# Optimization experiments

Hardware: AMD Instinct MI355X
Metric: run time of the kernel (lower is better)

Reference implementation:

```python
import jax, jax.numpy as jnp
import numpy as np

HEADS = 2
HID = 128
IN_DIM = 128
OUT_DIM = 1
N_NODES = 50000
NEG_SLOPE = 0.2  # PyG GATConv default
EPS = 1e-16


def setup_inputs() -> dict:
    key = jax.random.key(0)
    ks = jax.random.split(key, 16)
    N, E = N_NODES, 800000
    x = jax.random.normal(ks[0], (N, IN_DIM), dtype=jnp.float32)
    edge_index = jax.random.randint(ks[1], (2, E), 0, N, dtype=jnp.int32)
    s = 0.1
    # GATConv 1: in=128 -> heads=2, out=128 per head
    W1 = jax.random.normal(ks[2], (IN_DIM, HEADS * HID), dtype=jnp.float32) * s
    a_src1 = jax.random.normal(ks[3], (HEADS, HID), dtype=jnp.float32) * s
    a_dst1 = jax.random.normal(ks[4], (HEADS, HID), dtype=jnp.float32) * s
    b1 = jnp.zeros((HEADS * HID,), dtype=jnp.float32)
    # GATConv 2: in=256 -> heads=2, out=128 per head
    W2 = jax.random.normal(ks[5], (HEADS * HID, HEADS * HID), dtype=jnp.float32) * s
    a_src2 = jax.random.normal(ks[6], (HEADS, HID), dtype=jnp.float32) * s
    a_dst2 = jax.random.normal(ks[7], (HEADS, HID), dtype=jnp.float32) * s
    b2 = jnp.zeros((HEADS * HID,), dtype=jnp.float32)
    # post_mp: Linear(256,128) -> Dropout -> Linear(128,1)
    Wp1 = jax.random.normal(ks[8], (HEADS * HID, HID), dtype=jnp.float32) * s
    bp1 = jnp.zeros((HID,), dtype=jnp.float32)
    Wp2 = jax.random.normal(ks[9], (HID, OUT_DIM), dtype=jnp.float32) * s
    bp2 = jnp.zeros((OUT_DIM,), dtype=jnp.float32)
    return {"x": x, "edge_index": edge_index,
            "W1": W1, "a_src1": a_src1, "a_dst1": a_dst1, "b1": b1,
            "W2": W2, "a_src2": a_src2, "a_dst2": a_dst2, "b2": b2,
            "Wp1": Wp1, "bp1": bp1, "Wp2": Wp2, "bp2": bp2}


def gat_conv(x, src, dst, W, a_src, a_dst, b, num_nodes):
    """PyG-style GATConv (concat=True). src/dst already include self-loops."""
    N = num_nodes
    h = (x @ W).reshape(N, HEADS, HID)                        # [N,H,C]
    alpha_s = jnp.einsum('nhc,hc->nh', h, a_src)              # [N,H]
    alpha_d = jnp.einsum('nhc,hc->nh', h, a_dst)              # [N,H]
    e = jax.nn.leaky_relu(alpha_s[src] + alpha_d[dst], NEG_SLOPE)  # [E,H]
    # segment softmax over destination node
    emax = jax.ops.segment_max(e, dst, num_segments=N)        # [N,H]
    emax = jnp.where(jnp.isfinite(emax), emax, 0.0)
    w = jnp.exp(e - emax[dst])                                # [E,H]
    denom = jax.ops.segment_sum(w, dst, num_segments=N)       # [N,H]
    alpha = w / (denom[dst] + EPS)                            # [E,H]
    out = jax.ops.segment_sum(h[src] * alpha[:, :, None], dst, num_segments=N)
    return out.reshape(N, HEADS * HID) + b


def reference(x, edge_index, W1, a_src1, a_dst1, b1, W2, a_src2, a_dst2, b2,
              Wp1, bp1, Wp2, bp2):
    N = x.shape[0]
    loops = jnp.arange(N, dtype=edge_index.dtype)
    src = jnp.concatenate([edge_index[0], loops])
    dst = jnp.concatenate([edge_index[1], loops])
    h = gat_conv(x, src, dst, W1, a_src1, a_dst1, b1, N)
    h = jax.nn.relu(h)  # dropout is identity in eval mode
    h = gat_conv(h, src, dst, W2, a_src2, a_dst2, b2, N)
    h = jax.nn.relu(h)
    h = h @ Wp1 + bp1
    h = h @ Wp2 + bp2
    return jax.nn.sigmoid(h)
```

## Files before the change

kernel.cpp:

```cpp
#include <hip/hip_runtime.h>

#define HID 128
#define C2 256
#define NEG 0.2f
#define L2E 1.44269504088896340736f

typedef __bf16 v8bf __attribute__((ext_vector_type(8)));
typedef float  v4f  __attribute__((ext_vector_type(4)));
typedef float  v2f  __attribute__((ext_vector_type(2)));
typedef unsigned short us8 __attribute__((ext_vector_type(8)));

__device__ __forceinline__ float bf2f(unsigned short u) {
    union { float f; unsigned int i; } v; v.i = ((unsigned int)u) << 16; return v.f;
}
__device__ __forceinline__ unsigned short f2bf(float f) {
    union { float f; unsigned int i; } v; v.f = f;
    unsigned int r = v.i + 0x7FFFu + ((v.i >> 16) & 1u);
    return (unsigned short)(r >> 16);
}
__device__ __forceinline__ float lrelu(float x) { return x > 0.f ? x : NEG * x; }

__device__ __forceinline__ void packB_body(const float* __restrict__ W,
                                           unsigned short* __restrict__ out,
                                           int K, int N, int idx) {
    int ksteps = K >> 5;
    int total = (N >> 4) * ksteps * 64;
    if (idx >= total) return;
    int lane = idx & 63;
    int rest = idx >> 6;
    int tt = rest / ksteps, k0 = rest - tt * ksteps;
    int n = (tt >> 3) * 128 + (lane & 15) * 8 + (tt & 7);
    int kb = k0 * 32 + (lane >> 4) * 8;
    us8 v;
#pragma unroll
    for (int j = 0; j < 8; ++j) v[j] = f2bf(W[(size_t)(kb + j) * N + n]);
    *(us8*)(out + (size_t)idx * 8) = v;
}

__global__ __launch_bounds__(256) void prep_kernel(const float* __restrict__ W1, unsigned short* W1p,
                                                   const float* __restrict__ W2, unsigned short* W2p,
                                                   const float* __restrict__ Wp1, unsigned short* Wp1p,
                                                   const int* __restrict__ ei, int* __restrict__ cnt,
                                                   int* __restrict__ rank, int E,
                                                   int b1, int b2, int b3) {
    int b = blockIdx.x;
    if (b < b1) { packB_body(W1, W1p, HID, C2, b * 256 + threadIdx.x); return; }
    b -= b1;
    if (b < b2) { packB_body(W2, W2p, C2, C2, b * 256 + threadIdx.x); return; }
    b -= b2;
    if (b < b3) { packB_body(Wp1, Wp1p, C2, HID, b * 256 + threadIdx.x); return; }
    b -= b3;
    int i = b * 256 + threadIdx.x;
    if (i >= E) return;
    int d = ei[E + i];
    rank[i] = atomicAdd(&cnt[d], 1);
}

__global__ __launch_bounds__(256) void scanA(const int* __restrict__ cnt, int* __restrict__ rs,
                                             int* __restrict__ part, int N) {
    __shared__ int s[256];
    int t = threadIdx.x, i = blockIdx.x * 256 + t;
    int v = (i < N) ? cnt[i] : 0;
    s[t] = v; __syncthreads();
    for (int off = 1; off < 256; off <<= 1) {
        int x = (t >= off) ? s[t - off] : 0;
        __syncthreads();
        s[t] += x;
        __syncthreads();
    }
    if (i < N) rs[i] = s[t] - v;
    if (t == 255) part[blockIdx.x] = s[255];
}

__global__ __launch_bounds__(256) void scanB(int* __restrict__ part, int n) {
    __shared__ int s[256];
    int t = threadIdx.x;
    int v = (t < n) ? part[t] : 0;
    s[t] = v; __syncthreads();
    for (int off = 1; off < 256; off <<= 1) {
        int x = (t >= off) ? s[t - off] : 0;
        __syncthreads();
        s[t] += x;
        __syncthreads();
    }
    if (t < n) part[t] = s[t] - v;
}

__global__ void scanC(int* __restrict__ rs, const int* __restrict__ part, int N, int E) {
    int i = blockIdx.x * 256 + threadIdx.x;
    if (i < N) rs[i] += part[blockIdx.x];
    if (i == 0) rs[N] = E;
}

template<bool AFP32, int G, int KSTEPS>
__global__ __launch_bounds__(256) void gemm_alpha(const void* __restrict__ Av,
                                                  const unsigned short* __restrict__ Bp,
                                                  const float* __restrict__ asrc,
                                                  const float* __restrict__ adst,
                                                  float* __restrict__ asd,
                                                  unsigned char* __restrict__ C,
                                                  int M, int N, int gemmBlocks,
                                                  const int* __restrict__ ei,
                                                  const int* __restrict__ rs,
                                                  const int* __restrict__ rank,
                                                  int* __restrict__ csr, int E) {
    if (blockIdx.x >= gemmBlocks) {
        int i = (blockIdx.x - gemmBlocks) * 256 + threadIdx.x;
        if (i < E) {
            int s = ei[i], d = ei[E + i];
            csr[rs[d] + rank[i]] = s;
        }
        return;
    }
    constexpr int K = KSTEPS * 32;
    int ngrp = N >> 7;
    int mtiles = M >> 4;
    int w = (blockIdx.x << 2) + (threadIdx.x >> 6);
    int groups = (mtiles + G - 1) / G;
    int mp = w / ngrp, g = w - mp * ngrp;
    if (mp >= groups) return;
    int lane = threadIdx.x & 63;
    int l16 = lane & 15, quad = lane >> 4;
    int mt0 = mp * G;

    int mrow[G];
#pragma unroll
    for (int gi = 0; gi < G; ++gi) {
        int mt = mt0 + gi;
        mrow[gi] = (mt < mtiles ? mt : mtiles - 1) * 16 + l16;
    }

    const unsigned short* Bf = Bp + ((size_t)(g * 8) * KSTEPS << 9) + lane * 8;
    v4f acc[G][8];
#pragma unroll
    for (int gi = 0; gi < G; ++gi)
#pragma unroll
        for (int t = 0; t < 8; ++t) acc[gi][t] = (v4f){0, 0, 0, 0};

#pragma unroll
    for (int k0 = 0; k0 < KSTEPS; ++k0) {
        v8bf bfr[8];
#pragma unroll
        for (int t = 0; t < 8; ++t)
            bfr[t] = *(const v8bf*)(Bf + ((size_t)(t * KSTEPS + k0) << 9));
        v8bf a[G];
        if (AFP32) {
            const float* A = (const float*)Av;
#pragma unroll
            for (int gi = 0; gi < G; ++gi) {
                const float* p = A + (size_t)mrow[gi] * K + k0 * 32 + quad * 8;
                float4 u0 = *(const float4*)p, u1 = *(const float4*)(p + 4);
                a[gi][0]=(__bf16)u0.x; a[gi][1]=(__bf16)u0.y; a[gi][2]=(__bf16)u0.z; a[gi][3]=(__bf16)u0.w;
                a[gi][4]=(__bf16)u1.x; a[gi][5]=(__bf16)u1.y; a[gi][6]=(__bf16)u1.z; a[gi][7]=(__bf16)u1.w;
            }
        } else {
            const unsigned short* A = (const unsigned short*)Av;
#pragma unroll
            for (int gi = 0; gi < G; ++gi)
                a[gi] = *(const v8bf*)(A + (size_t)mrow[gi] * K + k0 * 32 + quad * 8);
        }
#pragma unroll
        for (int t = 0; t < 8; ++t)
#pragma unroll
            for (int gi = 0; gi < G; ++gi)
                acc[gi][t] = __builtin_amdgcn_mfma_f32_16x16x32_bf16(a[gi], bfr[t], acc[gi][t], 0, 0, 0);
    }

    int n0 = g << 7;
    int cb = n0 + l16 * 8;
    float sv[8], dv[8];
#pragma unroll
    for (int t = 0; t < 8; ++t) {
        sv[t] = asrc[cb + t];
        dv[t] = adst[cb + t];
    }
#pragma unroll
    for (int gi = 0; gi < G; ++gi) {
        int mt = mt0 + gi;
        if (mt >= mtiles) break;
        int row0 = mt * 16 + quad * 4;
#pragma unroll
        for (int r = 0; r < 4; ++r) {
            float sa = 0.f, sd = 0.f;
#pragma unroll
            for (int t = 0; t < 8; ++t) {
                sa += acc[gi][t][r] * sv[t];
                sd += acc[gi][t][r] * dv[t];
            }
            unsigned int w0 = __builtin_amdgcn_cvt_pk_fp8_f32(acc[gi][0][r], acc[gi][1][r], 0, false);
            w0 = __builtin_amdgcn_cvt_pk_fp8_f32(acc[gi][2][r], acc[gi][3][r], w0, true);
            unsigned int w1 = __builtin_amdgcn_cvt_pk_fp8_f32(acc[gi][4][r], acc[gi][5][r], 0, false);
            w1 = __builtin_amdgcn_cvt_pk_fp8_f32(acc[gi][6][r], acc[gi][7][r], w1, true);
            *(uint2*)(C + (size_t)(row0 + r) * N + cb) = (uint2){w0, w1};
#pragma unroll
            for (int off = 8; off; off >>= 1) {
                sa += __shfl_xor(sa, off);
                sd += __shfl_xor(sd, off);
            }
            if (l16 == 0) {
                int row = row0 + r;
                asd[(size_t)row * 4 + g]     = sa * L2E;
                asd[(size_t)row * 4 + 2 + g] = sd * L2E;
            }
        }
    }
}

__global__ __launch_bounds__(256) void agg_kernel(const int* __restrict__ rs,
                                                  const int* __restrict__ csr,
                                                  const unsigned char* __restrict__ h,
                                                  const float* __restrict__ asd,
                                                  const float* __restrict__ bias,
                                                  unsigned short* __restrict__ out, int N) {
    int d = blockIdx.x * 4 + (threadIdx.x >> 6);
    if (d >= N) return;
    int lane = threadIdx.x & 63;
    int beg = rs[d], end = rs[d + 1];
    int e4 = lane >> 4;
    int sub = lane & 15;
    int head = sub >> 3;
    int l32 = lane & 31;
    int whead = lane >> 5;
    float adh0 = asd[(size_t)d * 4 + 2];
    float adh1 = asd[(size_t)d * 4 + 3];
    float adh  = head  ? adh1 : adh0;
    float wadh = whead ? adh1 : adh0;
    int cbase = sub * 16;
    const unsigned char* hc = h + cbase;
    v2f acc[8];
#pragma unroll
    for (int j = 0; j < 8; ++j) acc[j] = (v2f){0, 0};
    float den = 0.f;
    for (int c0 = beg; c0 < end; c0 += 32) {
        int ce = c0 + l32;
        bool av = ce < end;
        int s_w = csr[av ? ce : end - 1];
        float e_w = lrelu(asd[(size_t)s_w * 4 + whead] + wadh);
        float w_w = av ? __builtin_amdgcn_exp2f(e_w) : 0.f;
        int rem = end - c0; if (rem > 32) rem = 32;
        int iters = (rem + 3) >> 2;
#pragma unroll 2
        for (int it = 0; it < iters; ++it) {
            int j = (it << 2) + e4;
            int   s   = __shfl(s_w, j);
            float wgt = __shfl(w_w, j + (head << 5));
            den += wgt;
            uint4 u = *(const uint4*)(hc + ((size_t)s << 8));
            v2f w2 = {wgt, wgt};
            acc[0] += w2 * __builtin_amdgcn_cvt_pk_f32_fp8(u.x, false);
            acc[1] += w2 * __builtin_amdgcn_cvt_pk_f32_fp8(u.x, true);
            acc[2] += w2 * __builtin_amdgcn_cvt_pk_f32_fp8(u.y, false);
            acc[3] += w2 * __builtin_amdgcn_cvt_pk_f32_fp8(u.y, true);
            acc[4] += w2 * __builtin_amdgcn_cvt_pk_f32_fp8(u.z, false);
            acc[5] += w2 * __builtin_amdgcn_cvt_pk_f32_fp8(u.z, true);
            acc[6] += w2 * __builtin_amdgcn_cvt_pk_f32_fp8(u.w, false);
            acc[7] += w2 * __builtin_amdgcn_cvt_pk_f32_fp8(u.w, true);
        }
    }
    float a[16];
#pragma unroll
    for (int j = 0; j < 8; ++j) { a[2 * j] = acc[j].x; a[2 * j + 1] = acc[j].y; }
#pragma unroll
    for (int j = 0; j < 16; ++j) a[j] += __shfl_xor(a[j], 16);
#pragma unroll
    for (int j = 0; j < 16; ++j) a[j] += __shfl_xor(a[j], 32);
    den += __shfl_xor(den, 16);
    den += __shfl_xor(den, 32);
    if (e4 == 0) {
        float wS = __builtin_amdgcn_exp2f(lrelu(asd[(size_t)d * 4 + head] + adh));
        uint4 u = *(const uint4*)(hc + (size_t)d * C2);
        v2f p;
        p = __builtin_amdgcn_cvt_pk_f32_fp8(u.x, false); a[0]  += wS * p.x; a[1]  += wS * p.y;
        p = __builtin_amdgcn_cvt_pk_f32_fp8(u.x, true);  a[2]  += wS * p.x; a[3]  += wS * p.y;
        p = __builtin_amdgcn_cvt_pk_f32_fp8(u.y, false); a[4]  += wS * p.x; a[5]  += wS * p.y;
        p = __builtin_amdgcn_cvt_pk_f32_fp8(u.y, true);  a[6]  += wS * p.x; a[7]  += wS * p.y;
        p = __builtin_amdgcn_cvt_pk_f32_fp8(u.z, false); a[8]  += wS * p.x; a[9]  += wS * p.y;
        p = __builtin_amdgcn_cvt_pk_f32_fp8(u.z, true);  a[10] += wS * p.x; a[11] += wS * p.y;
        p = __builtin_amdgcn_cvt_pk_f32_fp8(u.w, false); a[12] += wS * p.x; a[13] += wS * p.y;
        p = __builtin_amdgcn_cvt_pk_f32_fp8(u.w, true);  a[14] += wS * p.x; a[15] += wS * p.y;
        float rden = 1.f / (den + wS + 1e-16f);
        us8 o0, o1;
#pragma unroll
        for (int j = 0; j < 8; ++j) o0[j] = f2bf(fmaxf(a[j] * rden + bias[cbase + j], 0.f));
#pragma unroll
        for (int j = 0; j < 8; ++j) o1[j] = f2bf(fmaxf(a[8 + j] * rden + bias[cbase + 8 + j], 0.f));
        *(us8*)(out + (size_t)d * C2 + cbase) = o0;
        *(us8*)(out + (size_t)d * C2 + cbase + 8) = o1;
    }
}

template<int G, int KSTEPS>
__global__ __launch_bounds__(256) void gemm_final(const unsigned short* __restrict__ A,
                                                  const unsigned short* __restrict__ Bp,
                                                  const float* __restrict__ bp1,
                                                  const float* __restrict__ wp2,
                                                  const float* __restrict__ bp2,
                                                  float* __restrict__ out,
                                                  int M) {
    constexpr int K = KSTEPS * 32;
    int mtiles = M >> 4;
    int groups = (mtiles + G - 1) / G;
    int mp = (blockIdx.x << 2) + (threadIdx.x >> 6);
    if (mp >= groups) return;
    int lane = threadIdx.x & 63;
    int l16 = lane & 15, quad = lane >> 4;

    int mrow[G];
#pragma unroll
    for (int gi = 0; gi < G; ++gi) {
        int mt = mp * G + gi;
        mrow[gi] = (mt < mtiles ? mt : mtiles - 1) * 16 + l16;
    }

    const unsigned short* Bf = Bp + lane * 8;
    v4f acc[G][8];
#pragma unroll
    for (int gi = 0; gi < G; ++gi)
#pragma unroll
        for (int t = 0; t < 8; ++t) acc[gi][t] = (v4f){0, 0, 0, 0};
#pragma unroll
    for (int k0 = 0; k0 < KSTEPS; ++k0) {
        v8bf bfr[8];
#pragma unroll
        for (int t = 0; t < 8; ++t)
            bfr[t] = *(const v8bf*)(Bf + ((size_t)(t * KSTEPS + k0) << 9));
        v8bf a[G];
#pragma unroll
        for (int gi = 0; gi < G; ++gi)
            a[gi] = *(const v8bf*)(A + (size_t)mrow[gi] * K + k0 * 32 + quad * 8);
#pragma unroll
        for (int t = 0; t < 8; ++t)
#pragma unroll
            for (int gi = 0; gi < G; ++gi)
                acc[gi][t] = __builtin_amdgcn_mfma_f32_16x16x32_bf16(a[gi], bfr[t], acc[gi][t], 0, 0, 0);
    }
    int cb = l16 * 8;
    float wv8[8], bv[8];
#pragma unroll
    for (int t = 0; t < 8; ++t) {
        wv8[t] = wp2[cb + t];
        bv[t] = bp1[cb + t];
    }
    float bias2 = bp2[0];
#pragma unroll
    for (int gi = 0; gi < G; ++gi) {
        int mt = mp * G + gi;
        if (mt >= mtiles) break;
        int row0 = mt * 16 + quad * 4;
#pragma unroll
        for (int r = 0; r < 4; ++r) {
            float s = 0.f;
#pragma unroll
            for (int t = 0; t < 8; ++t) s += (acc[gi][t][r] + bv[t]) * wv8[t];
#pragma unroll
            for (int off = 8; off; off >>= 1) s += __shfl_xor(s, off);
            if (l16 == 0) {
                float xv = s + bias2;
                out[row0 + r] = 1.f / (1.f + __expf(-xv));
            }
        }
    }
}

extern "C" void kernel_launch(void* const* d_in, const int* in_sizes, int n_in,
                              void* d_out, int out_size, void* d_ws, size_t ws_size,
                              hipStream_t stream) {
    const float* x   = (const float*)d_in[0];
    const int*   ei  = (const int*)d_in[1];
    const float* W1  = (const float*)d_in[2];
    const float* as1 = (const float*)d_in[3];
    const float* ad1 = (const float*)d_in[4];
    const float* b1  = (const float*)d_in[5];
    const float* W2  = (const float*)d_in[6];
    const float* as2 = (const float*)d_in[7];
    const float* ad2 = (const float*)d_in[8];
    const float* b2  = (const float*)d_in[9];
    const float* Wp1 = (const float*)d_in[10];
    const float* bp1 = (const float*)d_in[11];
    const float* Wp2 = (const float*)d_in[12];
    const float* bp2 = (const float*)d_in[13];
    float* out = (float*)d_out;

    int NN = in_sizes[0] / HID;
    int E  = in_sizes[1] / 2;

    char* ws = (char*)d_ws;
    size_t off = 0;
    auto alloc = [&](size_t bytes) -> char* {
        char* p = ws + off;
        off += (bytes + 255) & ~(size_t)255;
        return p;
    };
    unsigned char*  bufH = (unsigned char*)alloc((size_t)NN * C2);
    unsigned short* bufO = (unsigned short*)alloc((size_t)NN * C2 * 2);
    float* asd = (float*)alloc((size_t)NN * 4 * sizeof(float));
    int* rs    = (int*)alloc((size_t)(NN + 1) * 4);
    int* cnt   = (int*)alloc((size_t)NN * 4);
    int* rank  = (int*)alloc((size_t)E * 4);
    int* csr   = (int*)alloc((size_t)E * 4);
    int* part  = (int*)alloc(1024);
    unsigned short* W1p  = (unsigned short*)alloc((size_t)HID * C2 * 2);
    unsigned short* W2p  = (unsigned short*)alloc((size_t)C2 * C2 * 2);
    unsigned short* Wp1p = (unsigned short*)alloc((size_t)C2 * HID * 2);

    int nchunk = (NN + 255) / 256;
    int eblk   = (E + 255) / 256;

    int pb1 = (HID * C2 / 8 + 255) / 256;
    int pb2 = (C2 * C2 / 8 + 255) / 256;
    int pb3 = (C2 * HID / 8 + 255) / 256;
    hipMemsetAsync(cnt, 0, (size_t)NN * 4, stream);
    prep_kernel<<<pb1 + pb2 + pb3 + eblk, 256, 0, stream>>>(W1, W1p, W2, W2p, Wp1, Wp1p,
                                                            ei, cnt, rank, E, pb1, pb2, pb3);
    scanA<<<nchunk, 256, 0, stream>>>(cnt, rs, part, NN);
    scanB<<<1, 256, 0, stream>>>(part, nchunk);
    scanC<<<nchunk, 256, 0, stream>>>(rs, part, NN, E);

    const int G = 2;
    int mtiles = NN / 16;
    int groups = (mtiles + G - 1) / G;
    int gemmBlocks = (groups * 2 + 3) / 4;
    int aggGrid = (NN + 3) / 4;

    gemm_alpha<true, G, 4><<<gemmBlocks + eblk, 256, 0, stream>>>(x, W1p, as1, ad1, asd, bufH,
                                                                  NN, C2, gemmBlocks,
                                                                  ei, rs, rank, csr, E);
    agg_kernel<<<aggGrid, 256, 0, stream>>>(rs, csr, bufH, asd, b1, bufO, NN);
    gemm_alpha<false, G, 8><<<gemmBlocks, 256, 0, stream>>>(bufO, W2p, as2, ad2, asd, bufH,
                                                            NN, C2, gemmBlocks,
                                                            nullptr, nullptr, nullptr, nullptr, 0);
    agg_kernel<<<aggGrid, 256, 0, stream>>>(rs, csr, bufH, asd, b2, bufO, NN);
    gemm_final<G, 8><<<(groups + 3) / 4, 256, 0, stream>>>(bufO, Wp1p, bp1, Wp2, bp2, out, NN);
}
```

Before: 305.9 us.

## Use 16 threads per destination node in GAT aggregation instead of a wavefront

The aggregation kernel now assigns 16 threads per destination node (16 nodes per block) instead of one 64-lane wavefront per node. Each thread walks the whole edge list serially, computing its head's edge weight directly, so the shuffle-based weight broadcast and cross-lane reduction are gone. This cuts redundant lanes and shuffle overhead for low-degree nodes (average degree about 17). In exchange there is less memory-level parallelism per node, per-edge index and score loads are repeated by all 16 threads, and divergence within a wavefront grows because four nodes of different degree share it.

```diff
diff --git a/kernel.cpp b/kernel.cpp
--- a/kernel.cpp
+++ b/kernel.cpp
@@ -212,81 +212,60 @@
                                                   const float* __restrict__ asd,
                                                   const float* __restrict__ bias,
                                                   unsigned short* __restrict__ out, int N) {
-    int d = blockIdx.x * 4 + (threadIdx.x >> 6);
+    int tid = threadIdx.x;
+    int grp = tid >> 4;
+    int sub = tid & 15;
+    int d = blockIdx.x * 16 + grp;
     if (d >= N) return;
-    int lane = threadIdx.x & 63;
+    int head = sub >> 3;
     int beg = rs[d], end = rs[d + 1];
-    int e4 = lane >> 4;
-    int sub = lane & 15;
-    int head = sub >> 3;
-    int l32 = lane & 31;
-    int whead = lane >> 5;
-    float adh0 = asd[(size_t)d * 4 + 2];
-    float adh1 = asd[(size_t)d * 4 + 3];
-    float adh  = head  ? adh1 : adh0;
-    float wadh = whead ? adh1 : adh0;
+    float adh = asd[(size_t)d * 4 + 2 + head];
     int cbase = sub * 16;
     const unsigned char* hc = h + cbase;
     v2f acc[8];
 #pragma unroll
     for (int j = 0; j < 8; ++j) acc[j] = (v2f){0, 0};
     float den = 0.f;
-    for (int c0 = beg; c0 < end; c0 += 32) {
-        int ce = c0 + l32;
-        bool av = ce < end;
-        int s_w = csr[av ? ce : end - 1];
-        float e_w = lrelu(asd[(size_t)s_w * 4 + whead] + wadh);
-        float w_w = av ? __builtin_amdgcn_exp2f(e_w) : 0.f;
-        int rem = end - c0; if (rem > 32) rem = 32;
-        int iters = (rem + 3) >> 2;
 #pragma unroll 2
-        for (int it = 0; it < iters; ++it) {
-            int j = (it << 2) + e4;
-            int   s   = __shfl(s_w, j);
-            float wgt = __shfl(w_w, j + (head << 5));
-            den += wgt;
-            uint4 u = *(const uint4*)(hc + ((size_t)s << 8));
-            v2f w2 = {wgt, wgt};
-            acc[0] += w2 * __builtin_amdgcn_cvt_pk_f32_fp8(u.x, false);
-            acc[1] += w2 * __builtin_amdgcn_cvt_pk_f32_fp8(u.x, true);
-            acc[2] += w2 * __builtin_amdgcn_cvt_pk_f32_fp8(u.y, false);
-            acc[3] += w2 * __builtin_amdgcn_cvt_pk_f32_fp8(u.y, true);
-            acc[4] += w2 * __builtin_amdgcn_cvt_pk_f32_fp8(u.z, false);
-            acc[5] += w2 * __builtin_amdgcn_cvt_pk_f32_fp8(u.z, true);
-            acc[6] += w2 * __builtin_amdgcn_cvt_pk_f32_fp8(u.w, false);
-            acc[7] += w2 * __builtin_amdgcn_cvt_pk_f32_fp8(u.w, true);
-        }
-    }
-    float a[16];
-#pragma unroll
-    for (int j = 0; j < 8; ++j) { a[2 * j] = acc[j].x; a[2 * j + 1] = acc[j].y; }
-#pragma unroll
-    for (int j = 0; j < 16; ++j) a[j] += __shfl_xor(a[j], 16);
-#pragma unroll
-    for (int j = 0; j < 16; ++j) a[j] += __shfl_xor(a[j], 32);
-    den += __shfl_xor(den, 16);
-    den += __shfl_xor(den, 32);
-    if (e4 == 0) {
-        float wS = __builtin_amdgcn_exp2f(lrelu(asd[(size_t)d * 4 + head] + adh));
-        uint4 u = *(const uint4*)(hc + (size_t)d * C2);
-        v2f p;
-        p = __builtin_amdgcn_cvt_pk_f32_fp8(u.x, false); a[0]  += wS * p.x; a[1]  += wS * p.y;
-        p = __builtin_amdgcn_cvt_pk_f32_fp8(u.x, true);  a[2]  += wS * p.x; a[3]  += wS * p.y;
-        p = __builtin_amdgcn_cvt_pk_f32_fp8(u.y, false); a[4]  += wS * p.x; a[5]  += wS * p.y;
-        p = __builtin_amdgcn_cvt_pk_f32_fp8(u.y, true);  a[6]  += wS * p.x; a[7]  += wS * p.y;
-        p = __builtin_amdgcn_cvt_pk_f32_fp8(u.z, false); a[8]  += wS * p.x; a[9]  += wS * p.y;
-        p = __builtin_amdgcn_cvt_pk_f32_fp8(u.z, true);  a[10] += wS * p.x; a[11] += wS * p.y;
-        p = __builtin_amdgcn_cvt_pk_f32_fp8(u.w, false); a[12] += wS * p.x; a[13] += wS * p.y;
-        p = __builtin_amdgcn_cvt_pk_f32_fp8(u.w, true);  a[14] += wS * p.x; a[15] += wS * p.y;
-        float rden = 1.f / (den + wS + 1e-16f);
-        us8 o0, o1;
-#pragma unroll
-        for (int j = 0; j < 8; ++j) o0[j] = f2bf(fmaxf(a[j] * rden + bias[cbase + j], 0.f));
-#pragma unroll
-        for (int j = 0; j < 8; ++j) o1[j] = f2bf(fmaxf(a[8 + j] * rden + bias[cbase + 8 + j], 0.f));
-        *(us8*)(out + (size_t)d * C2 + cbase) = o0;
-        *(us8*)(out + (size_t)d * C2 + cbase + 8) = o1;
-    }
+    for (int i = beg; i < end; ++i) {
+        int s = csr[i];
+        float wgt = __builtin_amdgcn_exp2f(lrelu(asd[(size_t)s * 4 + head] + adh));
+        den += wgt;
+        uint4 u = *(const uint4*)(hc + ((size_t)s << 8));
+        v2f w2 = {wgt, wgt};
+        acc[0] += w2 * __builtin_amdgcn_cvt_pk_f32_fp8(u.x, false);
+        acc[1] += w2 * __builtin_amdgcn_cvt_pk_f32_fp8(u.x, true);
+        acc[2] += w2 * __builtin_amdgcn_cvt_pk_f32_fp8(u.y, false);
+        acc[3] += w2 * __builtin_amdgcn_cvt_pk_f32_fp8(u.y, true);
+        acc[4] += w2 * __builtin_amdgcn_cvt_pk_f32_fp8(u.z, false);
+        acc[5] += w2 * __builtin_amdgcn_cvt_pk_f32_fp8(u.z, true);
+        acc[6] += w2 * __builtin_amdgcn_cvt_pk_f32_fp8(u.w, false);
+        acc[7] += w2 * __builtin_amdgcn_cvt_pk_f32_fp8(u.w, true);
+    }
+    float wS = __builtin_amdgcn_exp2f(lrelu(asd[(size_t)d * 4 + head] + adh));
+    {
+        uint4 u = *(const uint4*)(hc + ((size_t)d << 8));
+        v2f wsv = {wS, wS};
+        acc[0] += wsv * __builtin_amdgcn_cvt_pk_f32_fp8(u.x, false);
+        acc[1] += wsv * __builtin_amdgcn_cvt_pk_f32_fp8(u.x, true);
+        acc[2] += wsv * __builtin_amdgcn_cvt_pk_f32_fp8(u.y, false);
+        acc[3] += wsv * __builtin_amdgcn_cvt_pk_f32_fp8(u.y, true);
+        acc[4] += wsv * __builtin_amdgcn_cvt_pk_f32_fp8(u.z, false);
+        acc[5] += wsv * __builtin_amdgcn_cvt_pk_f32_fp8(u.z, true);
+        acc[6] += wsv * __builtin_amdgcn_cvt_pk_f32_fp8(u.w, false);
+        acc[7] += wsv * __builtin_amdgcn_cvt_pk_f32_fp8(u.w, true);
+    }
+    float rden = 1.f / (den + wS + 1e-16f);
+    us8 o0, o1;
+#pragma unroll
+    for (int j = 0; j < 4; ++j) {
+        o0[2 * j]     = f2bf(fmaxf(acc[j].x * rden + bias[cbase + 2 * j], 0.f));
+        o0[2 * j + 1] = f2bf(fmaxf(acc[j].y * rden + bias[cbase + 2 * j + 1], 0.f));
+        o1[2 * j]     = f2bf(fmaxf(acc[4 + j].x * rden + bias[cbase + 8 + 2 * j], 0.f));
+        o1[2 * j + 1] = f2bf(fmaxf(acc[4 + j].y * rden + bias[cbase + 8 + 2 * j + 1], 0.f));
+    }
+    *(us8*)(out + (size_t)d * C2 + cbase) = o0;
+    *(us8*)(out + (size_t)d * C2 + cbase + 8) = o1;
 }
 
 template<int G, int KSTEPS>
@@ -420,7 +399,7 @@
     int mtiles = NN / 16;
     int groups = (mtiles + G - 1) / G;
     int gemmBlocks = (groups * 2 + 3) / 4;
-    int aggGrid = (NN + 3) / 4;
+    int aggGrid = (NN + 15) / 16;
 
     gemm_alpha<true, G, 4><<<gemmBlocks + eblk, 256, 0, stream>>>(x, W1p, as1, ad1, asd, bufH,
                                                                   NN, C2, gemmBlocks,
```

Result: faster. 298.1 us (-2.6%).
